# Performance work log

Hardware: AMD Instinct MI355X
Metric: run time of the kernel (lower is better)

The kernel has to match this reference:

```python
import jax, jax.numpy as jnp
import numpy as np

HEADS = 8
NEG_SLOPE = 0.2
N_REL = 3
N_NODES = 10000
N_EDGES = 160000
OBS = 32
ACT = 8
N_GRAPHS = 16
HC = HEADS * OBS  # 256 = heads * out_channels (dim=1)


def _rgat_layer(x, w, q, k, e, we, b, src, dst, etype, eattr):
    """PyG RGATConv, additive-self-attention, across-relation, dim=1, concat=True, eval mode."""
    N = x.shape[0]
    # relation-specific transform for every node, then per-edge gather (avoids [E,in,out] bmm)
    xw = jnp.einsum('ni,rio->nro', x, w)              # [N, R, H*C]
    outi = xw[dst, etype]                              # [E, H*C] target features
    outj = xw[src, etype]                              # [E, H*C] source features
    alpha = outi @ q + outj @ k + (eattr @ we) @ e     # [E, H]
    alpha = jax.nn.leaky_relu(alpha, NEG_SLOPE)
    # segment softmax over destination neighborhoods (PyG softmax: detached max, +1e-16)
    amax = jax.lax.stop_gradient(jax.ops.segment_max(alpha, dst, num_segments=N))
    amax = jnp.where(jnp.isfinite(amax), amax, 0.0)
    ex = jnp.exp(alpha - amax[dst])
    denom = jax.ops.segment_sum(ex, dst, num_segments=N)
    attn = ex / (denom[dst] + 1e-16)                   # [E, H]
    E_ = outj.shape[0]
    msg = attn[:, :, None] * outj.reshape(E_, HEADS, -1)  # [E, H, C]
    agg = jax.ops.segment_sum(msg, dst, num_segments=N)   # [N, H, C]
    return agg.reshape(N, -1) + b                          # concat heads + bias


def setup_inputs() -> dict:
    key = jax.random.key(0)
    ks = jax.random.split(key, 32)
    s = 0.05
    inp = {
        'x': jax.random.normal(ks[0], (N_NODES, OBS), jnp.float32),
        'edge_index': jax.random.randint(ks[1], (2, N_EDGES), 0, N_NODES),
        'edge_type': jax.random.randint(ks[2], (N_EDGES,), 0, N_REL),
        'edge_attr': jax.random.normal(ks[3], (N_EDGES, 1), jnp.float32),
        'batch': jnp.sort(jax.random.randint(ks[4], (N_NODES,), 0, N_GRAPHS)),
    }
    ins = [OBS, HC, HC]
    i = 5
    for l, cin in enumerate(ins, start=1):
        inp[f'w{l}'] = s * jax.random.normal(ks[i + 0], (N_REL, cin, HC), jnp.float32)
        inp[f'q{l}'] = s * jax.random.normal(ks[i + 1], (HC, HEADS), jnp.float32)
        inp[f'k{l}'] = s * jax.random.normal(ks[i + 2], (HC, HEADS), jnp.float32)
        inp[f'e{l}'] = s * jax.random.normal(ks[i + 3], (HC, HEADS), jnp.float32)
        inp[f'we{l}'] = s * jax.random.normal(ks[i + 4], (1, HC), jnp.float32)
        inp[f'b{l}'] = jnp.zeros((HC,), jnp.float32)
        i += 5
    inp['wlin'] = s * jax.random.normal(ks[i], (HC, ACT), jnp.float32)
    inp['blin'] = jnp.zeros((ACT,), jnp.float32)
    return inp


def reference(x, edge_index, edge_type, edge_attr, batch,
              w1, q1, k1, e1, we1, b1,
              w2, q2, k2, e2, we2, b2,
              w3, q3, k3, e3, we3, b3,
              wlin, blin):
    src, dst = edge_index[0], edge_index[1]
    h = jax.nn.relu(_rgat_layer(x, w1, q1, k1, e1, we1, b1, src, dst, edge_type, edge_attr))
    h = jax.nn.relu(_rgat_layer(h, w2, q2, k2, e2, we2, b2, src, dst, edge_type, edge_attr))
    h = jax.nn.relu(_rgat_layer(h, w3, q3, k3, e3, we3, b3, src, dst, edge_type, edge_attr))
    h = jnp.tanh(h @ wlin + blin)                        # [N, ACT]
    sums = jax.ops.segment_sum(h, batch, num_segments=N_GRAPHS)
    cnts = jax.ops.segment_sum(jnp.ones((h.shape[0], 1), h.dtype), batch, num_segments=N_GRAPHS)
    return sums / jnp.maximum(cnts, 1.0)                 # global_mean_pool -> [G, ACT]
```

## Files before the change

### kernel.cpp

```cpp
#include <hip/hip_runtime.h>
#include <math.h>

#define HEADS 8
#define HC 256
#define NREL 3
#define NEG 0.2f
#define MAXDEG 128
#define PCHUNK 8
#define NCT 17

typedef float vfloat4 __attribute__((ext_vector_type(4)));
typedef short b16x8 __attribute__((ext_vector_type(8)));
typedef float f32x4 __attribute__((ext_vector_type(4)));

__device__ __forceinline__ float warp32_reduce(float p) {
#pragma unroll
    for (int off = 16; off > 0; off >>= 1) p += __shfl_down(p, off, 32);
    return p;
}

__device__ __forceinline__ unsigned short f2bf(float f) {
    unsigned u = __float_as_uint(f);
    unsigned r = (u + 0x7FFFu + ((u >> 16) & 1u)) >> 16;
    return (unsigned short)r;
}
__device__ __forceinline__ float bf2f(unsigned short b) {
    return __uint_as_float(((unsigned)b) << 16);
}


__global__ void k_init(int* deg, int* fill, int* ctr, int nnodes) {
    int i = blockIdx.x * blockDim.x + threadIdx.x;
    if (i < nnodes) { deg[i] = 0; fill[i] = 0; }
    if (i == 0) *ctr = 0;
}

__global__ void k_deg(const int* __restrict__ ei, int* deg, int nedges) {
    int e = blockIdx.x * blockDim.x + threadIdx.x;
    if (e < nedges) atomicAdd(&deg[ei[nedges + e]], 1);
}

__global__ void k_scan(const int* __restrict__ deg, int* rowptr, int n) {
    __shared__ int ss[1024];
    int tid = threadIdx.x;
    int per = (n + 1023) >> 10;
    int b = tid * per;
    int s = 0;
    for (int i = 0; i < per; i++) { int idx = b + i; if (idx < n) s += deg[idx]; }
    ss[tid] = s;
    __syncthreads();
    for (int off = 1; off < 1024; off <<= 1) {
        int v = (tid >= off) ? ss[tid - off] : 0;
        __syncthreads();
        ss[tid] += v;
        __syncthreads();
    }
    int run = (tid == 0) ? 0 : ss[tid - 1];
    for (int i = 0; i < per; i++) {
        int idx = b + i;
        if (idx < n) { rowptr[idx] = run; run += deg[idx]; }
    }
    if (tid == 0) rowptr[n] = ss[1023];
}

__global__ void k_scatter(const int* __restrict__ ei, const int* __restrict__ et,
                          const float* __restrict__ ea, const int* __restrict__ rowptr,
                          int* fill, int* csr_pack, float* csr_ae, int nedges) {
    int e = blockIdx.x * blockDim.x + threadIdx.x;
    if (e >= nedges) return;
    int dst = ei[nedges + e];
    int pos = atomicAdd(&fill[dst], 1);
    int slot = rowptr[dst] + pos;
    csr_pack[slot] = (ei[e] << 2) | (et[e] & 3);
    csr_ae[slot] = ea[e];
}

__global__ void k_wprep(
    const float* __restrict__ W1, const float* __restrict__ Q1, const float* __restrict__ K1,
    const float* __restrict__ E1, const float* __restrict__ WE1,
    const float* __restrict__ W2, const float* __restrict__ Q2, const float* __restrict__ K2,
    const float* __restrict__ E2, const float* __restrict__ WE2,
    const float* __restrict__ W3, const float* __restrict__ Q3, const float* __restrict__ K3,
    const float* __restrict__ E3, const float* __restrict__ WE3,
    unsigned short* __restrict__ b1hi, unsigned short* __restrict__ b1lo,
    unsigned short* __restrict__ b2hi, unsigned short* __restrict__ b2lo,
    unsigned short* __restrict__ b3hi, unsigned short* __restrict__ b3lo,
    float* __restrict__ wee,
    const float* __restrict__ x, unsigned short* __restrict__ x1hi,
    unsigned short* __restrict__ x1lo, int nnodes, int nprep) {
    int bi = blockIdx.x;
    int tid = threadIdx.x;
    if (bi >= nprep) {
        int i = (bi - nprep) * 256 + tid;
        if (i < nnodes * 32) {
            int n = i >> 5, k = i & 31;
            float f = x[i];
            unsigned short h = f2bf(f);
            int ntile = n >> 4, m = n & 15;
            int q = (k >> 3) & 3, j = k & 7;
            size_t o = ((size_t)ntile * 64 + q * 16 + m) * 8 + j;
            x1hi[o] = h;
            x1lo[o] = f2bf(f - bf2f(h));
        }
        return;
    }
    const float *w, *qm, *km, *em, *wem;
    unsigned short *bhi, *blo;
    int K, layer, lbi;
    if (bi < NREL * 32) {
        layer = 0; lbi = bi; K = 32;
        w = W1; qm = Q1; km = K1; em = E1; wem = WE1; bhi = b1hi; blo = b1lo;
    } else if (bi < NREL * 32 + NREL * HC) {
        layer = 1; lbi = bi - NREL * 32; K = HC;
        w = W2; qm = Q2; km = K2; em = E2; wem = WE2; bhi = b2hi; blo = b2lo;
    } else {
        layer = 2; lbi = bi - NREL * 32 - NREL * HC; K = HC;
        w = W3; qm = Q3; km = K3; em = E3; wem = WE3; bhi = b3hi; blo = b3lo;
    }
    int r = lbi / K, i = lbi - r * K;
    int KB = K / 32;
    int kb = i >> 5, qq = (i >> 3) & 3, j = i & 7;
    {
        int c = tid;
        float f = w[(size_t)lbi * HC + c];
        unsigned short h = f2bf(f);
        int ct = c >> 4, mc = c & 15;
        size_t o = ((((size_t)r * NCT + ct) * KB + kb) * 64 + qq * 16 + mc) * 8 + j;
        bhi[o] = h;
        blo[o] = f2bf(f - bf2f(h));
    }
    int h = tid >> 5, lane = tid & 31;
    const float* wrow = w + (size_t)lbi * HC;
    size_t base = (((size_t)r * NCT + 16) * KB + kb) * 512 + j;
    float p = 0.f;
    for (int o = lane; o < HC; o += 32) p += wrow[o] * qm[o * HEADS + h];
    p = warp32_reduce(p);
    if (lane == 0) {
        size_t o = base + (size_t)(qq * 16 + h) * 8;
        unsigned short hh = f2bf(p);
        bhi[o] = hh;
        blo[o] = f2bf(p - bf2f(hh));
    }
    p = 0.f;
    for (int o = lane; o < HC; o += 32) p += wrow[o] * km[o * HEADS + h];
    p = warp32_reduce(p);
    if (lane == 0) {
        size_t o = base + (size_t)(qq * 16 + 8 + h) * 8;
        unsigned short hh = f2bf(p);
        bhi[o] = hh;
        blo[o] = f2bf(p - bf2f(hh));
    }
    if (lbi == 0 && tid < HEADS) {
        float s = 0.f;
        for (int o = 0; o < HC; o++) s += wem[o] * em[o * HEADS + tid];
        wee[layer * HEADS + tid] = s;
    }
}

template <int K>
__global__ __launch_bounds__(256) void k_mfma(const unsigned short* __restrict__ pahi,
                                              const unsigned short* __restrict__ palo,
                                              const unsigned short* __restrict__ pbhi,
                                              const unsigned short* __restrict__ pblo,
                                              float* __restrict__ xw,
                                              float* __restrict__ qdot,
                                              float* __restrict__ kdot, int nnodes) {
    constexpr int KB = K / 32;
    int nt = blockIdx.x;
    int r = blockIdx.y;
    int t = threadIdx.x;
    int wv = t >> 6, lane = t & 63;
    int q = lane >> 4, m = lane & 15;
    const unsigned short* pa_hi = pahi + ((size_t)nt * KB * 64 + lane) * 8;
    const unsigned short* pa_lo = palo + ((size_t)nt * KB * 64 + lane) * 8;
    f32x4 acc[5] = {};
    for (int kb = 0; kb < KB; ++kb) {
        b16x8 ah = *(const b16x8*)(pa_hi + (size_t)kb * 512);
        b16x8 al = *(const b16x8*)(pa_lo + (size_t)kb * 512);
#pragma unroll
        for (int s = 0; s < 5; ++s) {
            int ct = wv + 4 * s;
            if (ct >= NCT) continue;
            size_t o = (((size_t)r * NCT + ct) * KB + kb) * 512 + (size_t)lane * 8;
            b16x8 vbh = *(const b16x8*)(pbhi + o);
            b16x8 vbl = *(const b16x8*)(pblo + o);
            acc[s] = __builtin_amdgcn_mfma_f32_16x16x32_bf16(ah, vbh, acc[s], 0, 0, 0);
            acc[s] = __builtin_amdgcn_mfma_f32_16x16x32_bf16(al, vbh, acc[s], 0, 0, 0);
            acc[s] = __builtin_amdgcn_mfma_f32_16x16x32_bf16(ah, vbl, acc[s], 0, 0, 0);
        }
    }
    int n0 = nt * 16;
#pragma unroll
    for (int s = 0; s < 5; ++s) {
        int ct = wv + 4 * s;
        if (ct >= NCT) continue;
        if (ct < 16) {
            int c = ct * 16 + m;
#pragma unroll
            for (int g = 0; g < 4; ++g) {
                int n = n0 + q * 4 + g;
                if (n < nnodes) xw[((size_t)n * NREL + r) * HC + c] = acc[s][g];
            }
        } else {
#pragma unroll
            for (int g = 0; g < 4; ++g) {
                int n = n0 + q * 4 + g;
                if (n < nnodes) {
                    if (m < 8) qdot[n * 24 + r * 8 + m] = acc[s][g];
                    else       kdot[n * 24 + r * 8 + (m - 8)] = acc[s][g];
                }
            }
        }
    }
}

__global__ __launch_bounds__(256) void k_agg(const float* __restrict__ xw,
                      const float* __restrict__ qdot, const float* __restrict__ kdot,
                      const int* __restrict__ rowptr, const int* __restrict__ csr_pack,
                      const float* __restrict__ csr_ae, const float* __restrict__ wee,
                      const float* __restrict__ bias, float* __restrict__ hout,
                      unsigned short* __restrict__ houthi, unsigned short* __restrict__ houtlo,
                      int nnodes) {
    __shared__ float salpha[4][MAXDEG * HEADS];
    __shared__ int spack[4][MAXDEG];
    int wv = threadIdx.x >> 6, lane = threadIdx.x & 63;
    int n = blockIdx.x * 4 + wv;
    if (n >= nnodes) return;
    int beg = rowptr[n];
    int deg = rowptr[n + 1] - beg;
    if (deg > MAXDEG) deg = MAXDEG;
    float* sal = salpha[wv];
    int* spk = spack[wv];
    {
        int h = lane & 7;
        float weeh = wee[h];
        const float* qdn = qdot + n * 24;
        for (int base = 0; base < deg; base += 8) {
            int d = base + (lane >> 3);
            if (d < deg) {
                int pk = csr_pack[beg + d];
                float ae = csr_ae[beg + d];
                int s = pk >> 2, t = pk & 3;
                if (h == 0) spk[d] = pk;
                float a = qdn[t * 8 + h] + kdot[s * 24 + t * 8 + h] + ae * weeh;
                sal[d * 8 + h] = (a > 0.f) ? a : NEG * a;
            }
        }
    }
    float sinv_h;
    {
        int h = lane & 7, c = lane >> 3;
        float m = -INFINITY;
        for (int d = c; d < deg; d += 8) m = fmaxf(m, sal[d * 8 + h]);
        m = fmaxf(m, __shfl_xor(m, 8, 64));
        m = fmaxf(m, __shfl_xor(m, 16, 64));
        m = fmaxf(m, __shfl_xor(m, 32, 64));
        float s = 0.f;
        for (int d = c; d < deg; d += 8) {
            float ex = expf(sal[d * 8 + h] - m);
            sal[d * 8 + h] = ex;
            s += ex;
        }
        s += __shfl_xor(s, 8, 64);
        s += __shfl_xor(s, 16, 64);
        s += __shfl_xor(s, 32, 64);
        sinv_h = 1.f / (s + 1e-16f);
    }
    float sinv_sel = __shfl(sinv_h, lane >> 3, 64);
    int hsel = lane >> 3;
    float4 acc4 = make_float4(0.f, 0.f, 0.f, 0.f);
    int d = 0;
    for (; d + 1 < deg; d += 2) {
        int pk0 = spk[d], pk1 = spk[d + 1];
        const float4* r0 = (const float4*)(xw + ((size_t)(pk0 >> 2) * NREL + (pk0 & 3)) * HC);
        const float4* r1 = (const float4*)(xw + ((size_t)(pk1 >> 2) * NREL + (pk1 & 3)) * HC);
        float4 v0 = r0[lane];
        float4 v1 = r1[lane];
        float a0 = sal[d * 8 + hsel];
        float a1 = sal[(d + 1) * 8 + hsel];
        acc4.x += a0 * v0.x + a1 * v1.x;
        acc4.y += a0 * v0.y + a1 * v1.y;
        acc4.z += a0 * v0.z + a1 * v1.z;
        acc4.w += a0 * v0.w + a1 * v1.w;
    }
    if (d < deg) {
        int pk = spk[d];
        const float4* r0 = (const float4*)(xw + ((size_t)(pk >> 2) * NREL + (pk & 3)) * HC);
        float4 v0 = r0[lane];
        float a0 = sal[d * 8 + hsel];
        acc4.x += a0 * v0.x;
        acc4.y += a0 * v0.y;
        acc4.z += a0 * v0.z;
        acc4.w += a0 * v0.w;
    }
    float4 bv = *(const float4*)(bias + lane * 4);
    float4 v;
    v.x = fmaxf(acc4.x * sinv_sel + bv.x, 0.f);
    v.y = fmaxf(acc4.y * sinv_sel + bv.y, 0.f);
    v.z = fmaxf(acc4.z * sinv_sel + bv.z, 0.f);
    v.w = fmaxf(acc4.w * sinv_sel + bv.w, 0.f);
    *(float4*)(hout + (size_t)n * HC + lane * 4) = v;
    int ntile = n >> 4, mm = n & 15;
    float vv[4] = {v.x, v.y, v.z, v.w};
#pragma unroll
    for (int i = 0; i < 4; ++i) {
        int c = lane * 4 + i;
        int kb = c >> 5, q = (c >> 3) & 3, j = c & 7;
        size_t o2 = ((((size_t)ntile * 8 + kb) * 64) + q * 16 + mm) * 8 + j;
        unsigned short hh = f2bf(vv[i]);
        houthi[o2] = hh;
        houtlo[o2] = f2bf(vv[i] - bf2f(hh));
    }
}

__global__ __launch_bounds__(256) void k_pool2(const float* __restrict__ h3,
                                               const float* __restrict__ wlin,
                                               const float* __restrict__ blin,
                                               const int* __restrict__ batch,
                                               float* __restrict__ partials,
                                               int* __restrict__ gcnt, int* __restrict__ ctr,
                                               float* __restrict__ out, int nnodes, int ngraph) {
    int g = blockIdx.x / PCHUNK, chunk = blockIdx.x % PCHUNK;
    __shared__ int sb[2];
    if (threadIdx.x < 2) {
        int target = g + threadIdx.x;
        int lo = 0, hi = nnodes;
        while (lo < hi) { int mid = (lo + hi) >> 1; if (batch[mid] < target) lo = mid + 1; else hi = mid; }
        sb[threadIdx.x] = lo;
    }
    __syncthreads();
    int beg = sb[0], end = sb[1];
    int t = threadIdx.x;
    int w = t >> 6, lane = t & 63;
    int h = lane & 7, grp = lane >> 3;
    float rw[32];
#pragma unroll
    for (int k = 0; k < 8; ++k)
#pragma unroll
        for (int j = 0; j < 4; ++j)
            rw[k * 4 + j] = wlin[(grp * 4 + j + 32 * k) * HEADS + h];
    float bl = blin[h];
    float acc = 0.f;
    int wg = chunk * 4 + w;
    for (int n = beg + wg; n < end; n += PCHUNK * 4) {
        const float* row = h3 + (size_t)n * HC;
        float dot = 0.f;
#pragma unroll
        for (int k = 0; k < 8; ++k) {
            float4 v = *(const float4*)&row[grp * 4 + 32 * k];
            dot += v.x * rw[k * 4] + v.y * rw[k * 4 + 1] + v.z * rw[k * 4 + 2] + v.w * rw[k * 4 + 3];
        }
        dot += __shfl_xor(dot, 8, 64);
        dot += __shfl_xor(dot, 16, 64);
        dot += __shfl_xor(dot, 32, 64);
        acc += tanhf(dot + bl);
    }
    __shared__ float sacc[4][HEADS];
    __shared__ float sred[HEADS];
    __shared__ int slast;
    if (lane < HEADS) sacc[w][h] = acc;
    __syncthreads();
    if (t < HEADS) sred[t] = sacc[0][t] + sacc[1][t] + sacc[2][t] + sacc[3][t];
    __syncthreads();
    if (t == 0) {
        for (int hh = 0; hh < HEADS; ++hh)
            partials[(size_t)blockIdx.x * HEADS + hh] = sred[hh];
        if (chunk == 0) gcnt[g] = end - beg;
        __threadfence();
        slast = (atomicAdd(ctr, 1) == (int)gridDim.x - 1);
    }
    __syncthreads();
    if (slast) {
        __threadfence();
        if (t < ngraph * HEADS) {
            int gg = t >> 3, hh = t & 7;
            float s = 0.f;
            for (int c = 0; c < PCHUNK; ++c)
                s += partials[(size_t)(gg * PCHUNK + c) * HEADS + hh];
            out[t] = s / fmaxf((float)gcnt[gg], 1.f);
        }
    }
}


extern "C" void kernel_launch(void* const* d_in, const int* in_sizes, int n_in,
                              void* d_out, int out_size, void* d_ws, size_t ws_size,
                              hipStream_t stream) {
    const float* x    = (const float*)d_in[0];
    const int*   ei   = (const int*)d_in[1];
    const int*   et   = (const int*)d_in[2];
    const float* ea   = (const float*)d_in[3];
    const int*   batch = (const int*)d_in[4];
    const float* W[3]  = {(const float*)d_in[5],  (const float*)d_in[11], (const float*)d_in[17]};
    const float* Q[3]  = {(const float*)d_in[6],  (const float*)d_in[12], (const float*)d_in[18]};
    const float* K[3]  = {(const float*)d_in[7],  (const float*)d_in[13], (const float*)d_in[19]};
    const float* Em[3] = {(const float*)d_in[8],  (const float*)d_in[14], (const float*)d_in[20]};
    const float* WE[3] = {(const float*)d_in[9],  (const float*)d_in[15], (const float*)d_in[21]};
    const float* B[3]  = {(const float*)d_in[10], (const float*)d_in[16], (const float*)d_in[22]};
    const float* wlin = (const float*)d_in[23];
    const float* blin = (const float*)d_in[24];

    int nnodes = in_sizes[0] / 32;
    int nedges = in_sizes[2];
    int ngraph = 16;
    int npad = (nnodes + 15) & ~15;

    char* ws = (char*)d_ws;
    size_t off = 0;
    auto alloc = [&](size_t bytes) -> void* {
        void* p = ws + off;
        off = (off + bytes + 255) & ~(size_t)255;
        return p;
    };
    int*   deg      = (int*)alloc((size_t)nnodes * 4);
    int*   fill     = (int*)alloc((size_t)nnodes * 4);
    int*   rowptr   = (int*)alloc((size_t)(nnodes + 1) * 4);
    int*   csr_pack = (int*)alloc((size_t)nedges * 4);
    float* csr_ae   = (float*)alloc((size_t)nedges * 4);
    float* xw       = (float*)alloc((size_t)npad * NREL * HC * 4);
    float* qdot     = (float*)alloc((size_t)npad * NREL * HEADS * 4);
    float* kdot     = (float*)alloc((size_t)npad * NREL * HEADS * 4);
    float* ha       = (float*)alloc((size_t)nnodes * HC * 4);
    float* hb       = (float*)alloc((size_t)nnodes * HC * 4);
    float* wee      = (float*)alloc((size_t)NREL * HEADS * 4);
    float* partials = (float*)alloc((size_t)ngraph * PCHUNK * HEADS * 4);
    int*   gcnt     = (int*)alloc((size_t)ngraph * 4);
    int*   ctr      = (int*)alloc(256);
    unsigned short* x1hi = (unsigned short*)alloc((size_t)npad * 32 * 2);
    unsigned short* x1lo = (unsigned short*)alloc((size_t)npad * 32 * 2);
    unsigned short* hahi = (unsigned short*)alloc((size_t)npad * HC * 2);
    unsigned short* halo = (unsigned short*)alloc((size_t)npad * HC * 2);
    unsigned short* hbhi = (unsigned short*)alloc((size_t)npad * HC * 2);
    unsigned short* hblo = (unsigned short*)alloc((size_t)npad * HC * 2);
    unsigned short* wt1hi = (unsigned short*)alloc((size_t)NREL * NCT * 1 * 512 * 2);
    unsigned short* wt1lo = (unsigned short*)alloc((size_t)NREL * NCT * 1 * 512 * 2);
    unsigned short* wt2hi = (unsigned short*)alloc((size_t)NREL * NCT * 8 * 512 * 2);
    unsigned short* wt2lo = (unsigned short*)alloc((size_t)NREL * NCT * 8 * 512 * 2);
    unsigned short* wt3hi = (unsigned short*)alloc((size_t)NREL * NCT * 8 * 512 * 2);
    unsigned short* wt3lo = (unsigned short*)alloc((size_t)NREL * NCT * 8 * 512 * 2);
    (void)ws_size; (void)n_in; (void)out_size;

    int nprep = NREL * 32 + 2 * NREL * HC;
    int npacka = (nnodes * 32 + 255) / 256;

    k_init<<<(nnodes + 255) / 256, 256, 0, stream>>>(deg, fill, ctr, nnodes);
    k_deg<<<(nedges + 255) / 256, 256, 0, stream>>>(ei, deg, nedges);
    k_scan<<<1, 1024, 0, stream>>>(deg, rowptr, nnodes);
    k_scatter<<<(nedges + 255) / 256, 256, 0, stream>>>(ei, et, ea, rowptr, fill, csr_pack, csr_ae, nedges);

    k_wprep<<<nprep + npacka, 256, 0, stream>>>(
        W[0], Q[0], K[0], Em[0], WE[0],
        W[1], Q[1], K[1], Em[1], WE[1],
        W[2], Q[2], K[2], Em[2], WE[2],
        wt1hi, wt1lo, wt2hi, wt2lo, wt3hi, wt3lo, wee,
        x, x1hi, x1lo, nnodes, nprep);

    dim3 gmfma((nnodes + 15) / 16, NREL);
    int gagg = (nnodes + 3) / 4;

    k_mfma<32><<<gmfma, 256, 0, stream>>>(x1hi, x1lo, wt1hi, wt1lo, xw, qdot, kdot, nnodes);
    k_agg<<<gagg, 256, 0, stream>>>(xw, qdot, kdot, rowptr, csr_pack, csr_ae, wee + 0, B[0], ha, hahi, halo, nnodes);

    k_mfma<HC><<<gmfma, 256, 0, stream>>>(hahi, halo, wt2hi, wt2lo, xw, qdot, kdot, nnodes);
    k_agg<<<gagg, 256, 0, stream>>>(xw, qdot, kdot, rowptr, csr_pack, csr_ae, wee + 8, B[1], hb, hbhi, hblo, nnodes);

    k_mfma<HC><<<gmfma, 256, 0, stream>>>(hbhi, hblo, wt3hi, wt3lo, xw, qdot, kdot, nnodes);
    k_agg<<<gagg, 256, 0, stream>>>(xw, qdot, kdot, rowptr, csr_pack, csr_ae, wee + 16, B[2], ha, hahi, halo, nnodes);

    k_pool2<<<ngraph * PCHUNK, 256, 0, stream>>>(ha, wlin, blin, batch, partials, gcnt, ctr,
                                                 (float*)d_out, nnodes, ngraph);
}
```

Measured before the change: 364.1 us.

## Replace CSR build with fixed-capacity per-node edge buckets fused into prep kernel

```diff
diff --git a/kernel.cpp b/kernel.cpp
--- a/kernel.cpp
+++ b/kernel.cpp
@@ -26,53 +26,6 @@
 }
 __device__ __forceinline__ float bf2f(unsigned short b) {
     return __uint_as_float(((unsigned)b) << 16);
-}
-
-
-__global__ void k_init(int* deg, int* fill, int* ctr, int nnodes) {
-    int i = blockIdx.x * blockDim.x + threadIdx.x;
-    if (i < nnodes) { deg[i] = 0; fill[i] = 0; }
-    if (i == 0) *ctr = 0;
-}
-
-__global__ void k_deg(const int* __restrict__ ei, int* deg, int nedges) {
-    int e = blockIdx.x * blockDim.x + threadIdx.x;
-    if (e < nedges) atomicAdd(&deg[ei[nedges + e]], 1);
-}
-
-__global__ void k_scan(const int* __restrict__ deg, int* rowptr, int n) {
-    __shared__ int ss[1024];
-    int tid = threadIdx.x;
-    int per = (n + 1023) >> 10;
-    int b = tid * per;
-    int s = 0;
-    for (int i = 0; i < per; i++) { int idx = b + i; if (idx < n) s += deg[idx]; }
-    ss[tid] = s;
-    __syncthreads();
-    for (int off = 1; off < 1024; off <<= 1) {
-        int v = (tid >= off) ? ss[tid - off] : 0;
-        __syncthreads();
-        ss[tid] += v;
-        __syncthreads();
-    }
-    int run = (tid == 0) ? 0 : ss[tid - 1];
-    for (int i = 0; i < per; i++) {
-        int idx = b + i;
-        if (idx < n) { rowptr[idx] = run; run += deg[idx]; }
-    }
-    if (tid == 0) rowptr[n] = ss[1023];
-}
-
-__global__ void k_scatter(const int* __restrict__ ei, const int* __restrict__ et,
-                          const float* __restrict__ ea, const int* __restrict__ rowptr,
-                          int* fill, int* csr_pack, float* csr_ae, int nedges) {
-    int e = blockIdx.x * blockDim.x + threadIdx.x;
-    if (e >= nedges) return;
-    int dst = ei[nedges + e];
-    int pos = atomicAdd(&fill[dst], 1);
-    int slot = rowptr[dst] + pos;
-    csr_pack[slot] = (ei[e] << 2) | (et[e] & 3);
-    csr_ae[slot] = ea[e];
 }
 
 __global__ void k_wprep(
@@ -87,9 +40,24 @@
     unsigned short* __restrict__ b3hi, unsigned short* __restrict__ b3lo,
     float* __restrict__ wee,
     const float* __restrict__ x, unsigned short* __restrict__ x1hi,
-    unsigned short* __restrict__ x1lo, int nnodes, int nprep) {
+    unsigned short* __restrict__ x1lo,
+    const int* __restrict__ ei, const int* __restrict__ et, const float* __restrict__ ea,
+    int* __restrict__ fill, int* __restrict__ bpack, float* __restrict__ bae,
+    int nnodes, int nedges, int nprep, int npacka) {
     int bi = blockIdx.x;
     int tid = threadIdx.x;
+    if (bi >= nprep + npacka) {
+        int e = (bi - nprep - npacka) * 256 + tid;
+        if (e < nedges) {
+            int dst = ei[nedges + e];
+            int pos = atomicAdd(&fill[dst], 1);
+            if (pos < MAXDEG) {
+                bpack[dst * MAXDEG + pos] = (ei[e] << 2) | (et[e] & 3);
+                bae[dst * MAXDEG + pos] = ea[e];
+            }
+        }
+        return;
+    }
     if (bi >= nprep) {
         int i = (bi - nprep) * 256 + tid;
         if (i < nnodes * 32) {
@@ -216,8 +184,8 @@
 
 __global__ __launch_bounds__(256) void k_agg(const float* __restrict__ xw,
                       const float* __restrict__ qdot, const float* __restrict__ kdot,
-                      const int* __restrict__ rowptr, const int* __restrict__ csr_pack,
-                      const float* __restrict__ csr_ae, const float* __restrict__ wee,
+                      const int* __restrict__ fill, const int* __restrict__ bpack,
+                      const float* __restrict__ bae, const float* __restrict__ wee,
                       const float* __restrict__ bias, float* __restrict__ hout,
                       unsigned short* __restrict__ houthi, unsigned short* __restrict__ houtlo,
                       int nnodes) {
@@ -226,8 +194,8 @@
     int wv = threadIdx.x >> 6, lane = threadIdx.x & 63;
     int n = blockIdx.x * 4 + wv;
     if (n >= nnodes) return;
-    int beg = rowptr[n];
-    int deg = rowptr[n + 1] - beg;
+    int beg = n * MAXDEG;
+    int deg = fill[n];
     if (deg > MAXDEG) deg = MAXDEG;
     float* sal = salpha[wv];
     int* spk = spack[wv];
@@ -238,8 +206,8 @@
         for (int base = 0; base < deg; base += 8) {
             int d = base + (lane >> 3);
             if (d < deg) {
-                int pk = csr_pack[beg + d];
-                float ae = csr_ae[beg + d];
+                int pk = bpack[beg + d];
+                float ae = bae[beg + d];
                 int s = pk >> 2, t = pk & 3;
                 if (h == 0) spk[d] = pk;
                 float a = qdn[t * 8 + h] + kdot[s * 24 + t * 8 + h] + ae * weeh;
@@ -412,11 +380,10 @@
         off = (off + bytes + 255) & ~(size_t)255;
         return p;
     };
-    int*   deg      = (int*)alloc((size_t)nnodes * 4);
-    int*   fill     = (int*)alloc((size_t)nnodes * 4);
-    int*   rowptr   = (int*)alloc((size_t)(nnodes + 1) * 4);
-    int*   csr_pack = (int*)alloc((size_t)nedges * 4);
-    float* csr_ae   = (float*)alloc((size_t)nedges * 4);
+    int*   fill     = (int*)alloc((size_t)(nnodes + 64) * 4);
+    int*   ctr      = fill + nnodes;
+    int*   bpack    = (int*)alloc((size_t)nnodes * MAXDEG * 4);
+    float* bae      = (float*)alloc((size_t)nnodes * MAXDEG * 4);
     float* xw       = (float*)alloc((size_t)npad * NREL * HC * 4);
     float* qdot     = (float*)alloc((size_t)npad * NREL * HEADS * 4);
     float* kdot     = (float*)alloc((size_t)npad * NREL * HEADS * 4);
@@ -425,7 +392,6 @@
     float* wee      = (float*)alloc((size_t)NREL * HEADS * 4);
     float* partials = (float*)alloc((size_t)ngraph * PCHUNK * HEADS * 4);
     int*   gcnt     = (int*)alloc((size_t)ngraph * 4);
-    int*   ctr      = (int*)alloc(256);
     unsigned short* x1hi = (unsigned short*)alloc((size_t)npad * 32 * 2);
     unsigned short* x1lo = (unsigned short*)alloc((size_t)npad * 32 * 2);
     unsigned short* hahi = (unsigned short*)alloc((size_t)npad * HC * 2);
@@ -442,30 +408,29 @@
 
     int nprep = NREL * 32 + 2 * NREL * HC;
     int npacka = (nnodes * 32 + 255) / 256;
-
-    k_init<<<(nnodes + 255) / 256, 256, 0, stream>>>(deg, fill, ctr, nnodes);
-    k_deg<<<(nedges + 255) / 256, 256, 0, stream>>>(ei, deg, nedges);
-    k_scan<<<1, 1024, 0, stream>>>(deg, rowptr, nnodes);
-    k_scatter<<<(nedges + 255) / 256, 256, 0, stream>>>(ei, et, ea, rowptr, fill, csr_pack, csr_ae, nedges);
-
-    k_wprep<<<nprep + npacka, 256, 0, stream>>>(
+    int nscat = (nedges + 255) / 256;
+
+    hipMemsetAsync(fill, 0, (size_t)(nnodes + 64) * 4, stream);
+    k_wprep<<<nprep + npacka + nscat, 256, 0, stream>>>(
         W[0], Q[0], K[0], Em[0], WE[0],
         W[1], Q[1], K[1], Em[1], WE[1],
         W[2], Q[2], K[2], Em[2], WE[2],
         wt1hi, wt1lo, wt2hi, wt2lo, wt3hi, wt3lo, wee,
-        x, x1hi, x1lo, nnodes, nprep);
+        x, x1hi, x1lo,
+        ei, et, ea, fill, bpack, bae,
+        nnodes, nedges, nprep, npacka);
 
     dim3 gmfma((nnodes + 15) / 16, NREL);
     int gagg = (nnodes + 3) / 4;
 
     k_mfma<32><<<gmfma, 256, 0, stream>>>(x1hi, x1lo, wt1hi, wt1lo, xw, qdot, kdot, nnodes);
-    k_agg<<<gagg, 256, 0, stream>>>(xw, qdot, kdot, rowptr, csr_pack, csr_ae, wee + 0, B[0], ha, hahi, halo, nnodes);
+    k_agg<<<gagg, 256, 0, stream>>>(xw, qdot, kdot, fill, bpack, bae, wee + 0, B[0], ha, hahi, halo, nnodes);
 
     k_mfma<HC><<<gmfma, 256, 0, stream>>>(hahi, halo, wt2hi, wt2lo, xw, qdot, kdot, nnodes);
-    k_agg<<<gagg, 256, 0, stream>>>(xw, qdot, kdot, rowptr, csr_pack, csr_ae, wee + 8, B[1], hb, hbhi, hblo, nnodes);
+    k_agg<<<gagg, 256, 0, stream>>>(xw, qdot, kdot, fill, bpack, bae, wee + 8, B[1], hb, hbhi, hblo, nnodes);
 
     k_mfma<HC><<<gmfma, 256, 0, stream>>>(hbhi, hblo, wt3hi, wt3lo, xw, qdot, kdot, nnodes);
-    k_agg<<<gagg, 256, 0, stream>>>(xw, qdot, kdot, rowptr, csr_pack, csr_ae, wee + 16, B[2], ha, hahi, halo, nnodes);
+    k_agg<<<gagg, 256, 0, stream>>>(xw, qdot, kdot, fill, bpack, bae, wee + 16, B[2], ha, hahi, halo, nnodes);
 
     k_pool2<<<ngraph * PCHUNK, 256, 0, stream>>>(ha, wlin, blin, batch, partials, gcnt, ctr,
                                                  (float*)d_out, nnodes, ngraph);
```

Measured after the change: 335.2 us. -7.9%, faster.
